# Performance work log

Measured on AMD Instinct MI355X. Metric: run time of the kernel, lower is better.

Reference implementation:

```python
import jax, jax.numpy as jnp
import numpy as np

ALPHA = 0.2  # LeakyReLU negative slope
NEG_INF = -9e15


def setup_inputs() -> dict:
    key = jax.random.key(0)
    k1, k2, k3, k4 = jax.random.split(key, 4)
    B, N, F_in, F_out = 8, 2048, 256, 128
    x = jax.random.normal(k1, (B, N, F_in), dtype=jnp.float32)
    adj = jax.random.randint(k2, (B, N, N), 0, 2, dtype=jnp.int32)
    # xavier-uniform-like init
    limW = float(np.sqrt(6.0 / (F_in + F_out)))
    W = jax.random.uniform(k3, (F_in, F_out), jnp.float32, -limW, limW)
    lima = float(np.sqrt(6.0 / (2 * F_out + 1)))
    a = jax.random.uniform(k4, (2 * F_out, 1), jnp.float32, -lima, lima)
    return {"x": x, "adj": adj, "W": W, "a": a}


def reference(x, adj, W, a):
    # x: [B, N, F_in], adj: [B, N, N], W: [F_in, F_out], a: [2*F_out, 1]
    F_out = W.shape[1]
    h = jnp.einsum('bnf,fo->bno', x, W)            # [B, N, F_out]
    a1 = a[:F_out, 0]                               # attends to source node i
    a2 = a[F_out:, 0]                               # attends to target node j
    f1 = h @ a1                                     # [B, N]
    f2 = h @ a2                                     # [B, N]
    # e[b,i,j] = leakyrelu(a1.h_i + a2.h_j) -- factored form of the concat trick
    e = jax.nn.leaky_relu(f1[:, :, None] + f2[:, None, :], negative_slope=ALPHA)
    attention = jnp.where(adj > 0, e, NEG_INF)
    attention = jax.nn.softmax(attention, axis=2)   # [B, N, N]
    # dropout is identity in eval mode
    h_prime = jnp.einsum('bij,bjo->bio', attention, h)  # [B, N, F_out]
    return jax.nn.elu(h_prime)                      # concat=True -> ELU
```

## Files before the change

### kernel.cpp

```cpp
#include <hip/hip_runtime.h>
#include <stdint.h>

#define BB   8
#define NN   2048
#define FIN  256
#define FOUT 128

using short8 = __attribute__((ext_vector_type(8))) short;
using f32x4  = __attribute__((ext_vector_type(4))) float;

__device__ __forceinline__ unsigned short rbf(float f) {
    return (unsigned short)((__float_as_uint(f) + 0x8000u) >> 16);
}

__device__ __forceinline__ void mfma_calib(int m, int quad, int* Mlab, int* Nlab) {
    short8 pa1, pb1, pa2, pb2;
    const short one = (short)0x3F80;
    const short mb  = (short)rbf((float)m);
#pragma unroll
    for (int j = 0; j < 8; ++j) { pa1[j] = 0; pa2[j] = 0; pb1[j] = mb; pb2[j] = one; }
    if (quad == 0) { pa1[0] = one; pa2[0] = mb; }
    f32x4 zz = {0.f, 0.f, 0.f, 0.f};
    f32x4 c1 = __builtin_amdgcn_mfma_f32_16x16x32_bf16(pa1, pb1, zz, 0, 0, 0);
    f32x4 c2 = __builtin_amdgcn_mfma_f32_16x16x32_bf16(pa2, pb2, zz, 0, 0, 0);
#pragma unroll
    for (int r = 0; r < 4; ++r) {
        Nlab[r] = ((int)c1[r]) & 15;
        Mlab[r] = ((int)c2[r]) & 15;
    }
}

__global__ __launch_bounds__(256) void gat_wt(const float* __restrict__ W,
                                              unsigned short* __restrict__ wt) {
    const int g  = blockIdx.x * 256 + threadIdx.x;
    const int k  = g >> 5;
    const int o4 = (g & 31) << 2;
    float4 wv = *(const float4*)(W + (k << 7) + o4);
    wt[((o4 + 0) << 8) + k] = rbf(wv.x);
    wt[((o4 + 1) << 8) + k] = rbf(wv.y);
    wt[((o4 + 2) << 8) + k] = rbf(wv.z);
    wt[((o4 + 3) << 8) + k] = rbf(wv.w);
}

__global__ __launch_bounds__(256) void gat_bm(const int* __restrict__ adj,
                                              unsigned char* __restrict__ bm) {
    const int row = blockIdx.x;
    const int tid = threadIdx.x;
    const int4* p = (const int4*)(adj + ((size_t)row << 11) + (tid << 3));
    int4 a0 = p[0];
    int4 a1 = p[1];
    unsigned int b = (unsigned int)(a0.x > 0)
                   | ((unsigned int)(a0.y > 0) << 1)
                   | ((unsigned int)(a0.z > 0) << 2)
                   | ((unsigned int)(a0.w > 0) << 3)
                   | ((unsigned int)(a1.x > 0) << 4)
                   | ((unsigned int)(a1.y > 0) << 5)
                   | ((unsigned int)(a1.z > 0) << 6)
                   | ((unsigned int)(a1.w > 0) << 7);
    bm[(row << 8) + tid] = (unsigned char)b;
}

__global__ __launch_bounds__(256) void gat_h3(
        const float* __restrict__ x, const unsigned short* __restrict__ wt,
        const float* __restrict__ a, unsigned short* __restrict__ ht,
        float* __restrict__ f1, float* __restrict__ f2) {
    __shared__ unsigned short xs[16][264];
    __shared__ float hs[16][132];
    const int bk   = blockIdx.x;
    const int R0   = bk << 4;
    const int b    = R0 >> 11;
    const int il0  = R0 & (NN - 1);
    const int tid  = threadIdx.x;
    const int w    = tid >> 6;
    const int lane = tid & 63;
    const int m    = lane & 15;
    const int quad = lane >> 4;

#pragma unroll
    for (int rr = 0; rr < 4; ++rr) {
        const int row = (w << 2) + rr;
        float4 xv = *(const float4*)(x + (size_t)(R0 + row) * FIN + (lane << 2));
        ushort4 c4;
        c4.x = rbf(xv.x); c4.y = rbf(xv.y); c4.z = rbf(xv.z); c4.w = rbf(xv.w);
        *(ushort4*)(&xs[row][lane << 2]) = c4;
    }
    int Mlab[4], Nlab[4];
    mfma_calib(m, quad, Mlab, Nlab);
    __syncthreads();

    f32x4 zz = {0.f, 0.f, 0.f, 0.f};
    f32x4 acc[2] = {zz, zz};
#pragma unroll
    for (int kc = 0; kc < 8; ++kc) {
        const int k0 = (kc << 5) + (quad << 3);
        short8 av = *(const short8*)(&xs[m][k0]);
#pragma unroll
        for (int t = 0; t < 2; ++t) {
            const int ot = (w << 1) + t;
            short8 bw = *(const short8*)(wt + (((ot << 4) + m) << 8) + k0);
            acc[t] = __builtin_amdgcn_mfma_f32_16x16x32_bf16(av, bw, acc[t], 0, 0, 0);
        }
    }
#pragma unroll
    for (int t = 0; t < 2; ++t)
#pragma unroll
        for (int r = 0; r < 4; ++r)
            hs[Mlab[r]][(((w << 1) + t) << 4) + Nlab[r]] = acc[t][r];
    __syncthreads();

    {
        const int i   = tid >> 4;
        const int seg = tid & 15;
        const int o0  = seg << 3;
        float s1 = 0.f, s2 = 0.f;
#pragma unroll
        for (int e = 0; e < 8; ++e) {
            float hv = hs[i][o0 + e];
            s1 = fmaf(hv, a[o0 + e], s1);
            s2 = fmaf(hv, a[FOUT + o0 + e], s2);
        }
        s1 += __shfl_xor(s1, 1); s1 += __shfl_xor(s1, 2);
        s1 += __shfl_xor(s1, 4); s1 += __shfl_xor(s1, 8);
        s2 += __shfl_xor(s2, 1); s2 += __shfl_xor(s2, 2);
        s2 += __shfl_xor(s2, 4); s2 += __shfl_xor(s2, 8);
        if (seg == 0) { f1[R0 + i] = s1; f2[R0 + i] = s2; }
    }
    {
        const int o  = tid >> 1;
        const int i8 = (tid & 1) << 3;
        short8 hv;
#pragma unroll
        for (int e = 0; e < 8; ++e) hv[e] = (short)rbf(hs[i8 + e][o]);
        *(short8*)(ht + ((size_t)((b << 7) + o) << 11) + il0 + i8) = hv;
    }
}

#define LOADC(H, MskA, MskB, Fa, Fb, c) { \
    const int j0_ = jb + ((c) << 5); \
    _Pragma("unroll") \
    for (int ot = 0; ot < 8; ++ot) \
        H[ot] = *(const short8*)(htb + ((size_t)((ot << 4) + m) << 11) + j0_); \
    MskA = bmr0[mbb + ((c) << 2)]; \
    MskB = bmr1[mbb + ((c) << 2)]; \
    Fa = *(const float4*)(f2b + j0_); \
    Fb = *(const float4*)(f2b + j0_ + 4); \
}

#define COMPC(H, MskA, MskB, Fa, Fb) { \
    float fm_[8] = {Fa.x, Fa.y, Fa.z, Fa.w, Fb.x, Fb.y, Fb.z, Fb.w}; \
    float pA_[8], pB_[8]; \
    _Pragma("unroll") \
    for (int u = 0; u < 8; ++u) { \
        float e = f1a + fm_[u]; \
        pA_[u] = (MskA & (1u << u)) ? __expf(fmaxf(e, 0.2f * e)) : 0.f; \
    } \
    _Pragma("unroll") \
    for (int u = 0; u < 8; ++u) { \
        float e = f1b + fm_[u]; \
        pB_[u] = (MskB & (1u << u)) ? __expf(fmaxf(e, 0.2f * e)) : 0.f; \
    } \
    s1 += ((pA_[0]+pA_[1])+(pA_[2]+pA_[3]))+((pA_[4]+pA_[5])+(pA_[6]+pA_[7])); \
    s2 += ((pB_[0]+pB_[1])+(pB_[2]+pB_[3]))+((pB_[4]+pB_[5])+(pB_[6]+pB_[7])); \
    short8 pf1_, pf2_; \
    _Pragma("unroll") \
    for (int u = 0; u < 8; ++u) { pf1_[u] = (short)rbf(pA_[u]); pf2_[u] = (short)rbf(pB_[u]); } \
    _Pragma("unroll") \
    for (int ot = 0; ot < 8; ++ot) { \
        acc1[ot] = __builtin_amdgcn_mfma_f32_16x16x32_bf16(pf1_, H[ot], acc1[ot], 0, 0, 0); \
        acc2[ot] = __builtin_amdgcn_mfma_f32_16x16x32_bf16(pf2_, H[ot], acc2[ot], 0, 0, 0); \
    } \
}

__global__ __launch_bounds__(256, 2) void gat_s5(
        const unsigned char* __restrict__ bm, const unsigned short* __restrict__ ht,
        const float* __restrict__ f1, const float* __restrict__ f2,
        float* __restrict__ out) {
    const int bk   = blockIdx.x;
    const int b    = bk & 7;
    const int i0   = (bk >> 3) << 5;
    const int tid  = threadIdx.x;
    const int w    = tid >> 6;
    const int lane = tid & 63;
    const int m    = lane & 15;
    const int quad = lane >> 4;

    __shared__ float accb[2][32][128];
    __shared__ float sbuf[4][2][16];

    const int gi0 = (b << 11) + i0;
    const float f1a = f1[gi0 + m];
    const float f1b = f1[gi0 + 16 + m];
    const unsigned char* bmr0 = bm + ((size_t)(gi0 + m) << 8);
    const unsigned char* bmr1 = bm + ((size_t)(gi0 + 16 + m) << 8);
    const float* f2b = f2 + (b << 11);
    const unsigned short* htb = ht + ((size_t)b << 18);

    const int jb  = (w << 9) + (quad << 3);
    const int mbb = (w << 6) + quad;

    f32x4 zz = {0.f, 0.f, 0.f, 0.f};
    f32x4 acc1[8], acc2[8];
#pragma unroll
    for (int t = 0; t < 8; ++t) { acc1[t] = zz; acc2[t] = zz; }
    float s1 = 0.f, s2 = 0.f;

    short8 hfA[8], hfB[8];
    unsigned int mA0, mB0, mA1, mB1;
    float4 faA, fbA, faB, fbB;

    LOADC(hfA, mA0, mB0, faA, fbA, 0);
    for (int cc = 0; cc < 7; ++cc) {
        const int c0 = cc << 1;
        LOADC(hfB, mA1, mB1, faB, fbB, c0 + 1);
        COMPC(hfA, mA0, mB0, faA, fbA);
        LOADC(hfA, mA0, mB0, faA, fbA, c0 + 2);
        COMPC(hfB, mA1, mB1, faB, fbB);
    }
    LOADC(hfB, mA1, mB1, faB, fbB, 15);
    COMPC(hfA, mA0, mB0, faA, fbA);
    COMPC(hfB, mA1, mB1, faB, fbB);

    s1 += __shfl_xor(s1, 16); s1 += __shfl_xor(s1, 32);
    s2 += __shfl_xor(s2, 16); s2 += __shfl_xor(s2, 32);
    if (lane < 16) { sbuf[w][0][lane] = s1; sbuf[w][1][lane] = s2; }

    int Mlab[4], Nlab[4];
    mfma_calib(m, quad, Mlab, Nlab);

    if (w < 2) {
#pragma unroll
        for (int ot = 0; ot < 8; ++ot)
#pragma unroll
            for (int r = 0; r < 4; ++r) {
                accb[w][Mlab[r]][(ot << 4) + Nlab[r]]      = acc1[ot][r];
                accb[w][16 + Mlab[r]][(ot << 4) + Nlab[r]] = acc2[ot][r];
            }
    }
    __syncthreads();
    if (w >= 2) {
#pragma unroll
        for (int ot = 0; ot < 8; ++ot)
#pragma unroll
            for (int r = 0; r < 4; ++r) {
                accb[w - 2][Mlab[r]][(ot << 4) + Nlab[r]]      += acc1[ot][r];
                accb[w - 2][16 + Mlab[r]][(ot << 4) + Nlab[r]] += acc2[ot][r];
            }
    }
    __syncthreads();

    {
        const int row = tid >> 3;
        const int o0  = (tid & 7) << 4;
        const int g   = row >> 4;
        const int mm  = row & 15;
        const float s = (sbuf[0][g][mm] + sbuf[1][g][mm]) +
                        (sbuf[2][g][mm] + sbuf[3][g][mm]);
        const float inv = 1.0f / s;
        float* orow = out + (((size_t)gi0 + row) << 7) + o0;
#pragma unroll
        for (int v4 = 0; v4 < 4; ++v4) {
            float4 rv;
            float y;
            y = (accb[0][row][o0 + 4 * v4 + 0] + accb[1][row][o0 + 4 * v4 + 0]) * inv;
            rv.x = y > 0.f ? y : expm1f(y);
            y = (accb[0][row][o0 + 4 * v4 + 1] + accb[1][row][o0 + 4 * v4 + 1]) * inv;
            rv.y = y > 0.f ? y : expm1f(y);
            y = (accb[0][row][o0 + 4 * v4 + 2] + accb[1][row][o0 + 4 * v4 + 2]) * inv;
            rv.z = y > 0.f ? y : expm1f(y);
            y = (accb[0][row][o0 + 4 * v4 + 3] + accb[1][row][o0 + 4 * v4 + 3]) * inv;
            rv.w = y > 0.f ? y : expm1f(y);
            *(float4*)(orow + 4 * v4) = rv;
        }
    }
}

extern "C" void kernel_launch(void* const* d_in, const int* in_sizes, int n_in,
                              void* d_out, int out_size, void* d_ws, size_t ws_size,
                              hipStream_t stream) {
    const float* x   = nullptr;
    const int*   adj = nullptr;
    const float* W   = nullptr;
    const float* a   = nullptr;
    for (int i = 0; i < n_in; ++i) {
        const long s = in_sizes[i];
        if      (s == (long)BB * NN * NN)  adj = (const int*)d_in[i];
        else if (s == (long)BB * NN * FIN) x   = (const float*)d_in[i];
        else if (s == (long)FIN * FOUT)    W   = (const float*)d_in[i];
        else if (s == 2L * FOUT)           a   = (const float*)d_in[i];
    }
    if (!x)   x   = (const float*)d_in[0];
    if (!adj) adj = (const int*)d_in[1];
    if (!W)   W   = (const float*)d_in[2];
    if (!a)   a   = (const float*)d_in[3];
    float* out = (float*)d_out;

    unsigned short* wt = (unsigned short*)d_ws;
    unsigned short* ht = wt + 32768;
    float* f1  = (float*)(ht + (size_t)BB * NN * FOUT);
    float* f2  = f1 + BB * NN;
    unsigned char* bmw = (unsigned char*)(f2 + BB * NN);

    hipLaunchKernelGGL(gat_wt,  dim3(32),    dim3(256), 0, stream, W, wt);
    hipLaunchKernelGGL(gat_bm,  dim3(16384), dim3(256), 0, stream, adj, bmw);
    hipLaunchKernelGGL(gat_h3,  dim3(1024),  dim3(256), 0, stream, x, wt, a, ht, f1, f2);
    hipLaunchKernelGGL(gat_s5,  dim3(512),   dim3(256), 0, stream, bmw, ht, f1, f2, out);
}
```

Baseline: 261.6 us.

## Reorder bitmask and bf16 h layouts to match MFMA fragment access

The adjacency bitmask and the transposed bf16 h buffer are now written in a tiled layout that matches how each wave in the attention kernel reads them. Each lane's H fragment load becomes a contiguous 16-byte read at lane<<3 inside a 4 KB chunk, and mask bytes for 32 rows sit next to each other. Before, these were strided reads across 2048-element rows. The aim is coalesced global loads in the main loop, paid for by scattered byte stores in the bitmask kernel and more complex address math in the producer kernels.

```diff
diff --git a/kernel.cpp b/kernel.cpp
--- a/kernel.cpp
+++ b/kernel.cpp
@@ -42,8 +42,8 @@
     wt[((o4 + 3) << 8) + k] = rbf(wv.w);
 }
 
-__global__ __launch_bounds__(256) void gat_bm(const int* __restrict__ adj,
-                                              unsigned char* __restrict__ bm) {
+__global__ __launch_bounds__(256) void gat_bm2(const int* __restrict__ adj,
+                                               unsigned char* __restrict__ bm) {
     const int row = blockIdx.x;
     const int tid = threadIdx.x;
     const int4* p = (const int4*)(adj + ((size_t)row << 11) + (tid << 3));
@@ -57,10 +57,12 @@
                    | ((unsigned int)(a1.y > 0) << 5)
                    | ((unsigned int)(a1.z > 0) << 6)
                    | ((unsigned int)(a1.w > 0) << 7);
-    bm[(row << 8) + tid] = (unsigned char)b;
-}
-
-__global__ __launch_bounds__(256) void gat_h3(
+    const int w = tid >> 6, c = (tid >> 2) & 15, q = tid & 3;
+    bm[((size_t)(row >> 5) << 13) + (c << 9) + (w << 7) + (q << 5) + (row & 31)]
+        = (unsigned char)b;
+}
+
+__global__ __launch_bounds__(256) void gat_h4(
         const float* __restrict__ x, const unsigned short* __restrict__ wt,
         const float* __restrict__ a, unsigned short* __restrict__ ht,
         float* __restrict__ f1, float* __restrict__ f2) {
@@ -128,20 +130,27 @@
     {
         const int o  = tid >> 1;
         const int i8 = (tid & 1) << 3;
+        const int jj = il0 + i8;
+        const int wj = jj >> 9;
+        const int cj = (jj >> 5) & 15;
+        const int qj = (jj >> 3) & 3;
         short8 hv;
 #pragma unroll
         for (int e = 0; e < 8; ++e) hv[e] = (short)rbf(hs[i8 + e][o]);
-        *(short8*)(ht + ((size_t)((b << 7) + o) << 11) + il0 + i8) = hv;
+        const size_t addr = ((size_t)b << 18) + ((size_t)wj << 16) + (cj << 12)
+                          + ((o >> 4) << 9) + (((qj << 4) + (o & 15)) << 3);
+        *(short8*)(ht + addr) = hv;
     }
 }
 
 #define LOADC(H, MskA, MskB, Fa, Fb, c) { \
+    const unsigned short* hp_ = htb + ((c) << 12); \
+    _Pragma("unroll") \
+    for (int ot = 0; ot < 8; ++ot) \
+        H[ot] = *(const short8*)(hp_ + (ot << 9) + (lane << 3)); \
+    MskA = bmb[((c) << 9) + mq]; \
+    MskB = bmb[((c) << 9) + mq + 16]; \
     const int j0_ = jb + ((c) << 5); \
-    _Pragma("unroll") \
-    for (int ot = 0; ot < 8; ++ot) \
-        H[ot] = *(const short8*)(htb + ((size_t)((ot << 4) + m) << 11) + j0_); \
-    MskA = bmr0[mbb + ((c) << 2)]; \
-    MskB = bmr1[mbb + ((c) << 2)]; \
     Fa = *(const float4*)(f2b + j0_); \
     Fb = *(const float4*)(f2b + j0_ + 4); \
 }
@@ -171,7 +180,7 @@
     } \
 }
 
-__global__ __launch_bounds__(256, 2) void gat_s5(
+__global__ __launch_bounds__(256, 2) void gat_s6(
         const unsigned char* __restrict__ bm, const unsigned short* __restrict__ ht,
         const float* __restrict__ f1, const float* __restrict__ f2,
         float* __restrict__ out) {
@@ -190,13 +199,12 @@
     const int gi0 = (b << 11) + i0;
     const float f1a = f1[gi0 + m];
     const float f1b = f1[gi0 + 16 + m];
-    const unsigned char* bmr0 = bm + ((size_t)(gi0 + m) << 8);
-    const unsigned char* bmr1 = bm + ((size_t)(gi0 + 16 + m) << 8);
+    const unsigned char* bmb = bm + ((size_t)gi0 << 8);
+    const int mq = (w << 7) + (quad << 5) + m;
     const float* f2b = f2 + (b << 11);
-    const unsigned short* htb = ht + ((size_t)b << 18);
+    const unsigned short* htb = ht + ((size_t)b << 18) + ((size_t)w << 16);
 
     const int jb  = (w << 9) + (quad << 3);
-    const int mbb = (w << 6) + quad;
 
     f32x4 zz = {0.f, 0.f, 0.f, 0.f};
     f32x4 acc1[8], acc2[8];
@@ -301,7 +309,7 @@
     unsigned char* bmw = (unsigned char*)(f2 + BB * NN);
 
     hipLaunchKernelGGL(gat_wt,  dim3(32),    dim3(256), 0, stream, W, wt);
-    hipLaunchKernelGGL(gat_bm,  dim3(16384), dim3(256), 0, stream, adj, bmw);
-    hipLaunchKernelGGL(gat_h3,  dim3(1024),  dim3(256), 0, stream, x, wt, a, ht, f1, f2);
-    hipLaunchKernelGGL(gat_s5,  dim3(512),   dim3(256), 0, stream, bmw, ht, f1, f2, out);
-}
+    hipLaunchKernelGGL(gat_bm2, dim3(16384), dim3(256), 0, stream, adj, bmw);
+    hipLaunchKernelGGL(gat_h4,  dim3(1024),  dim3(256), 0, stream, x, wt, a, ht, f1, f2);
+    hipLaunchKernelGGL(gat_s6,  dim3(512),   dim3(256), 0, stream, bmw, ht, f1, f2, out);
+}
```

Result: faster. 239.8 us (median of 3 runs) (-8.3%).
